# Performance work log

Hardware: AMD Instinct MI355X
Metric: run time of the kernel (lower is better)

Reference implementation:

```python
import jax, jax.numpy as jnp
import numpy as np

S_MIN = 0.01
S_MAX = 36500.0
SEQ_LEN = 128
BATCH = 65536


def setup_inputs() -> dict:
    key = jax.random.key(0)
    k1, k2 = jax.random.split(key)
    # elapsed days: nonnegative floats; ratings: integers 1..4 stored as float
    t = jax.random.uniform(k1, (SEQ_LEN, BATCH), dtype=jnp.float32) * 30.0
    rating = jax.random.randint(k2, (SEQ_LEN, BATCH), 1, 5).astype(jnp.float32)
    inputs = jnp.stack([t, rating], axis=-1)  # [S, B, 2]
    w = jnp.array([0.4, 0.6, 2.4, 5.8, 4.93, 0.94, 0.86, 0.01, 1.49,
                   0.14, 0.94, 2.18, 0.05, 0.34, 1.26, 0.29, 2.61],
                  dtype=jnp.float32)
    return {"inputs": inputs, "w": w}


def _first_step(X, w):
    # state is all-zeros only on the first step (clamp keeps s >= S_MIN after)
    rating = X[:, 1]
    ridx = jnp.clip(rating.astype(jnp.int32) - 1, 0, 3)
    valid = (rating >= 1) & (rating <= 4)
    new_s = jnp.where(valid, w[ridx], 1.0)
    new_d = jnp.clip(w[4] - w[5] * (rating - 3.0), 1.0, 10.0)
    new_s = jnp.clip(new_s, S_MIN, S_MAX)
    return jnp.stack([new_s, new_d], axis=1)  # [B, 2]


def _step(w, state, X):
    s, d = state[:, 0], state[:, 1]
    t, rating = X[:, 0], X[:, 1]
    # power forgetting curve: r = (1 + t / (9 s))^-1
    r = 1.0 / (1.0 + t / (9.0 * s))
    hard_penalty = jnp.where(rating == 2, w[15], 1.0)
    easy_bonus = jnp.where(rating == 4, w[16], 1.0)
    s_success = s * (1.0 + jnp.exp(w[8]) * (11.0 - d) * jnp.power(s, -w[9])
                     * (jnp.exp((1.0 - r) * w[10]) - 1.0)
                     * hard_penalty * easy_bonus)
    s_failure = jnp.minimum(
        w[11] * jnp.power(d, -w[12]) * (jnp.power(s + 1.0, w[13]) - 1.0)
        * jnp.exp((1.0 - r) * w[14]),
        s)
    new_s = jnp.where(rating > 1.0, s_success, s_failure)
    new_d = d - w[6] * (rating - 3.0)
    new_d = w[7] * w[4] + (1.0 - w[7]) * new_d  # mean reversion to w[4]
    new_d = jnp.clip(new_d, 1.0, 10.0)
    new_s = jnp.clip(new_s, S_MIN, S_MAX)
    new_state = jnp.stack([new_s, new_d], axis=1)
    return new_state, new_state


def reference(inputs, w):
    state0 = _first_step(inputs[0], w)  # [B, 2]
    final_state, rest = jax.lax.scan(lambda st, X: _step(w, st, X),
                                     state0, inputs[1:])
    outputs = jnp.concatenate([state0[None], rest], axis=0)  # [S, B, 2]
    return outputs, final_state
```

## Files before the change

### kernel.cpp

```cpp
#include <hip/hip_runtime.h>

#define BATCH_N 65536
#define SEQ_N   128

typedef float v2f __attribute__((ext_vector_type(2)));

__global__ __launch_bounds__(256, 1) void fsrs_kernel(
    const v2f* __restrict__ in,
    const float* __restrict__ w,
    v2f*       __restrict__ out)
{
    const int b = blockIdx.x * 256 + threadIdx.x;

    const float w0 = w[0], w1 = w[1], w2 = w[2], w3 = w[3];
    const float w4 = w[4], w5 = w[5], w6 = w[6], w7 = w[7];
    const float w9 = w[9], w11 = w[11], w12 = w[12], w13 = w[13];
    const float w15 = w[15], w16 = w[16];
    constexpr float LOG2E = 1.44269504088896340736f;
    const float w8l  = w[8]  * LOG2E;
    const float w10l = w[10] * LOG2E;
    const float w14l = w[14] * LOG2E;
    const float omw7   = 1.0f - w7;
    const float omw7w6 = omw7 * w6;
    const float dc0    = w7 * w4 + 3.0f * omw7w6;

    const v2f* ip = in  + b;
    v2f*       op = out + b;

    float s = 0.01f;
    float dpre = 1.0f;

    v2f rawA[16], rawB[16];
    float tX[16], dX[16], mX[16];
    float tY[16], dY[16], mY[16];

    auto loadC = [&](v2f* raw, int base) {
#pragma unroll
        for (int i = 0; i < 16; ++i) raw[i] = ip[(base + i) * BATCH_N];
    };

    auto preC = [&](const v2f* raw, float* T, float* D, float* M, int lo) {
#pragma unroll
        for (int i = 0; i < 16; ++i) {
            if (i < lo) continue;
            const float tt = raw[i].x, rating = raw[i].y;
            const float hb = (rating == 2.0f) ? w15
                           : ((rating == 4.0f) ? w16 : 1.0f);
            const float eh = (11.0f - dpre) * hb;
            const float m2 = w11 * __builtin_amdgcn_exp2f(
                                 -w12 * __builtin_amdgcn_logf(dpre));
            M[i] = (rating > 1.0f) ? eh : -m2;
            const float nd = __builtin_fmaf(omw7, dpre,
                              __builtin_fmaf(-omw7w6, rating, dc0));
            dpre = fminf(fmaxf(nd, 1.0f), 10.0f);
            T[i] = tt;
            D[i] = dpre;
        }
    };

    auto stepRow = [&](float tt, float ms, float dd, int row) {
        const bool  sel = ms > 0.0f;
        const float q   = __builtin_fmaf(9.0f, s, tt);
        const float omr = tt * __builtin_amdgcn_rcpf(q);
        const float e   = __builtin_amdgcn_exp2f(omr * (sel ? w10l : w14l));
        const float ls  = __builtin_amdgcn_logf(sel ? s : (s + 1.0f));
        const float aa  = sel ? __builtin_fmaf(-w9, ls, w8l) : (w13 * ls);
        const float A   = __builtin_amdgcn_exp2f(aa);
        const float Af  = sel ? A          : (A - 1.0f);
        const float Ef  = sel ? (e - 1.0f) : e;
        const float m   = sel ? (ms * s)   : (-ms);
        const float P   = Af * Ef * m;
        const float su  = fminf(s + P, 36500.0f);
        const float fl  = fmaxf(fminf(P, s), 0.01f);
        s = sel ? su : fl;
        v2f o; o.x = s; o.y = dd;
        __builtin_nontemporal_store(o, &op[row * BATCH_N]);
    };

    auto phase = [&](const float* T, const float* D, const float* M,
                     int base, int lo, v2f* raw, int loadBase, bool doLoad) {
#pragma unroll
        for (int q = 0; q < 4; ++q) {
            if (doLoad) {
#pragma unroll
                for (int j = 0; j < 4; ++j)
                    raw[4 * q + j] = ip[(loadBase + 4 * q + j) * BATCH_N];
            }
#pragma unroll
            for (int j = 0; j < 4; ++j) {
                const int i = 4 * q + j;
                if (i < lo) continue;
                stepRow(T[i], M[i], D[i], base + i);
            }
        }
    };

    loadC(rawA, 0);
    loadC(rawB, 16);

    const float r0 = rawA[0].y;
    {
        const float d0 = fminf(fmaxf(
            __builtin_fmaf(-w5, r0 - 3.0f, w4), 1.0f), 10.0f);
        dpre = d0;
        tX[0] = rawA[0].x; dX[0] = d0; mX[0] = 1.0f;
    }
    preC(rawA, tX, dX, mX, 1);

    {
        const float wsel = (r0 < 2.5f) ? ((r0 < 1.5f) ? w0 : w1)
                                       : ((r0 < 3.5f) ? w2 : w3);
        const float ns = (r0 >= 1.0f && r0 <= 4.0f) ? wsel : 1.0f;
        s = fminf(fmaxf(ns, 0.01f), 36500.0f);
        v2f o; o.x = s; o.y = dX[0];
        __builtin_nontemporal_store(o, &op[0]);
    }
    phase(tX, dX, mX, 0, 1, rawA, 32, true);
    preC(rawB, tY, dY, mY, 0);
    phase(tY, dY, mY, 16, 0, rawB, 48, true);

#pragma unroll 1
    for (int c = 0; c < 2; ++c) {
        preC(rawA, tX, dX, mX, 0);
        phase(tX, dX, mX, 32 * (c + 1), 0,
              rawA, 32 * (c + 2), true);
        preC(rawB, tY, dY, mY, 0);
        phase(tY, dY, mY, 32 * (c + 1) + 16, 0,
              rawB, 32 * (c + 2) + 16, true);
    }

    preC(rawA, tX, dX, mX, 0);
    phase(tX, dX, mX, 96, 0, rawA, 0, false);
    preC(rawB, tY, dY, mY, 0);
    phase(tY, dY, mY, 112, 0, rawB, 0, false);

    {
        v2f o; o.x = s; o.y = dY[15];
        op[SEQ_N * BATCH_N] = o;
    }
}

extern "C" void kernel_launch(void* const* d_in, const int* in_sizes, int n_in,
                              void* d_out, int out_size, void* d_ws, size_t ws_size,
                              hipStream_t stream) {
    const v2f*   in = (const v2f*)d_in[0];
    const float* w  = (const float*)d_in[1];
    v2f* out = (v2f*)d_out;
    fsrs_kernel<<<BATCH_N / 256, 256, 0, stream>>>(in, w, out);
}
```

Baseline: 113.7 us.

## Interleave difficulty precompute with serial stability steps and merge exponentials

Restructures the per-thread pipeline so the independent difficulty/multiplier precompute for the next 16-row chunk runs row by row alongside the serial stability recurrence of the current chunk, and loads are issued in the same loop. The dependent chain can then be hidden behind independent ALU work instead of running precompute as a separate serial block. It also rewrites the stability update algebraically as a difference of two exp2 terms, (u - v) * m, which removes a multiply and a subtract from the critical path but can lose precision when u and v are close. The schedule is more intricate and raises register pressure.

```diff
diff --git a/kernel.cpp b/kernel.cpp
--- a/kernel.cpp
+++ b/kernel.cpp
@@ -39,37 +39,32 @@
         for (int i = 0; i < 16; ++i) raw[i] = ip[(base + i) * BATCH_N];
     };
 
-    auto preC = [&](const v2f* raw, float* T, float* D, float* M, int lo) {
-#pragma unroll
-        for (int i = 0; i < 16; ++i) {
-            if (i < lo) continue;
-            const float tt = raw[i].x, rating = raw[i].y;
-            const float hb = (rating == 2.0f) ? w15
-                           : ((rating == 4.0f) ? w16 : 1.0f);
-            const float eh = (11.0f - dpre) * hb;
-            const float m2 = w11 * __builtin_amdgcn_exp2f(
-                                 -w12 * __builtin_amdgcn_logf(dpre));
-            M[i] = (rating > 1.0f) ? eh : -m2;
-            const float nd = __builtin_fmaf(omw7, dpre,
-                              __builtin_fmaf(-omw7w6, rating, dc0));
-            dpre = fminf(fmaxf(nd, 1.0f), 10.0f);
-            T[i] = tt;
-            D[i] = dpre;
-        }
+    auto preRow = [&](v2f r, float* T, float* D, float* M, int i) {
+        const float tt = r.x, rating = r.y;
+        const float hb = (rating == 2.0f) ? w15
+                       : ((rating == 4.0f) ? w16 : 1.0f);
+        const float eh = (11.0f - dpre) * hb;
+        const float m2 = w11 * __builtin_amdgcn_exp2f(
+                             -w12 * __builtin_amdgcn_logf(dpre));
+        M[i] = (rating > 1.0f) ? eh : -m2;
+        const float nd = __builtin_fmaf(omw7, dpre,
+                          __builtin_fmaf(-omw7w6, rating, dc0));
+        dpre = fminf(fmaxf(nd, 1.0f), 10.0f);
+        T[i] = tt;
+        D[i] = dpre;
     };
 
     auto stepRow = [&](float tt, float ms, float dd, int row) {
         const bool  sel = ms > 0.0f;
         const float q   = __builtin_fmaf(9.0f, s, tt);
         const float omr = tt * __builtin_amdgcn_rcpf(q);
-        const float e   = __builtin_amdgcn_exp2f(omr * (sel ? w10l : w14l));
+        const float x   = omr * (sel ? w10l : w14l);
         const float ls  = __builtin_amdgcn_logf(sel ? s : (s + 1.0f));
         const float aa  = sel ? __builtin_fmaf(-w9, ls, w8l) : (w13 * ls);
-        const float A   = __builtin_amdgcn_exp2f(aa);
-        const float Af  = sel ? A          : (A - 1.0f);
-        const float Ef  = sel ? (e - 1.0f) : e;
-        const float m   = sel ? (ms * s)   : (-ms);
-        const float P   = Af * Ef * m;
+        const float u   = __builtin_amdgcn_exp2f(aa + x);
+        const float v   = __builtin_amdgcn_exp2f(sel ? aa : x);
+        const float m   = sel ? (ms * s) : (-ms);
+        const float P   = (u - v) * m;
         const float su  = fminf(s + P, 36500.0f);
         const float fl  = fmaxf(fminf(P, s), 0.01f);
         s = sel ? su : fl;
@@ -77,21 +72,23 @@
         __builtin_nontemporal_store(o, &op[row * BATCH_N]);
     };
 
-    auto phase = [&](const float* T, const float* D, const float* M,
-                     int base, int lo, v2f* raw, int loadBase, bool doLoad) {
+    auto preC = [&](const v2f* raw, float* T, float* D, float* M, int lo) {
 #pragma unroll
-        for (int q = 0; q < 4; ++q) {
-            if (doLoad) {
+        for (int i = 0; i < 16; ++i) {
+            if (i < lo) continue;
+            preRow(raw[i], T, D, M, i);
+        }
+    };
+
+    auto fused = [&](const float* T, const float* D, const float* M,
+                     int sb, int lo,
+                     const v2f* rawSrc, float* T2, float* D2, float* M2,
+                     bool doPre, v2f* rawDst, int lb, bool doLoad) {
 #pragma unroll
-                for (int j = 0; j < 4; ++j)
-                    raw[4 * q + j] = ip[(loadBase + 4 * q + j) * BATCH_N];
-            }
-#pragma unroll
-            for (int j = 0; j < 4; ++j) {
-                const int i = 4 * q + j;
-                if (i < lo) continue;
-                stepRow(T[i], M[i], D[i], base + i);
-            }
+        for (int i = 0; i < 16; ++i) {
+            if (doLoad) rawDst[i] = ip[(lb + i) * BATCH_N];
+            if (doPre)  preRow(rawSrc[i], T2, D2, M2, i);
+            if (i >= lo) stepRow(T[i], M[i], D[i], sb + i);
         }
     };
 
@@ -115,24 +112,18 @@
         v2f o; o.x = s; o.y = dX[0];
         __builtin_nontemporal_store(o, &op[0]);
     }
-    phase(tX, dX, mX, 0, 1, rawA, 32, true);
-    preC(rawB, tY, dY, mY, 0);
-    phase(tY, dY, mY, 16, 0, rawB, 48, true);
+
+    fused(tX, dX, mX, 0, 1, rawB, tY, dY, mY, true, rawA, 32, true);
 
 #pragma unroll 1
-    for (int c = 0; c < 2; ++c) {
-        preC(rawA, tX, dX, mX, 0);
-        phase(tX, dX, mX, 32 * (c + 1), 0,
-              rawA, 32 * (c + 2), true);
-        preC(rawB, tY, dY, mY, 0);
-        phase(tY, dY, mY, 32 * (c + 1) + 16, 0,
-              rawB, 32 * (c + 2) + 16, true);
+    for (int c = 0; c < 3; ++c) {
+        fused(tY, dY, mY, 16 * (2 * c + 1), 0,
+              rawA, tX, dX, mX, true, rawB, 16 * (2 * c + 3), true);
+        fused(tX, dX, mX, 16 * (2 * c + 2), 0,
+              rawB, tY, dY, mY, true, rawA, 16 * (2 * c + 4), c < 2);
     }
 
-    preC(rawA, tX, dX, mX, 0);
-    phase(tX, dX, mX, 96, 0, rawA, 0, false);
-    preC(rawB, tY, dY, mY, 0);
-    phase(tY, dY, mY, 112, 0, rawB, 0, false);
+    fused(tY, dY, mY, 112, 0, rawA, tX, dX, mX, false, rawB, 0, false);
 
     {
         v2f o; o.x = s; o.y = dY[15];
```

After: 113.1 us, median of 2. Within noise of the previous version (-0.5%).
